# Kernel tuning notes

Measured on AMD Instinct MI355X. Metric: run time of the kernel, lower is better.

Reference implementation:

```python
import jax, jax.numpy as jnp
import numpy as np

DIM = 4096
BATCH = 64
DEFAULT_LR = 0.001
DEFAULT_ALPHA = 0.01
EPS = 1e-08


def setup_inputs() -> dict:
    key = jax.random.key(0)
    k1, k2, k3 = jax.random.split(key, 3)
    weight = jax.random.normal(k1, (DIM, DIM), dtype=jnp.float32)
    input_x = jax.random.normal(k2, (BATCH, DIM), dtype=jnp.float32)
    grad = jax.random.normal(k3, (DIM, DIM), dtype=jnp.float32)
    return {"weight": weight, "input_x": input_x, "grad": grad}


def reference(weight, input_x, grad):
    # L2-normalize inputs along last dim (normalize_inputs=True)
    x = input_x / (jnp.linalg.norm(input_x, axis=-1, keepdims=True) + EPS)
    # batched outer product averaged over batch: (dim, dim)
    outer = jnp.einsum('bi,bj->ij', x, x) / x.shape[0]
    decay_matrix = jnp.eye(DIM, dtype=weight.dtype) - DEFAULT_ALPHA * outer
    # W_{t+1} = W @ (I - alpha * outer) - lr * grad
    new_weight = weight @ decay_matrix - DEFAULT_LR * grad
    return new_weight
```

## Files before the change

kernel.cpp:

```cpp
#include <hip/hip_runtime.h>
#include <math.h>

#define DIM 4096
#define BATCH 64

typedef __attribute__((ext_vector_type(8))) short short8;
typedef __attribute__((ext_vector_type(4))) float f32x4;

__device__ __forceinline__ float4 ld4(const float* p) {
    return *reinterpret_cast<const float4*>(p);
}

__device__ __forceinline__ unsigned short f2bf(float f) {
    unsigned u = __builtin_bit_cast(unsigned, f);
    u = (u + 0x7fffu + ((u >> 16) & 1u)) >> 16;
    return (unsigned short)u;
}

__global__ __launch_bounds__(256) void k_norm(const float* __restrict__ x,
                                              unsigned short* __restrict__ xb1,
                                              unsigned short* __restrict__ xb2) {
    const int b = blockIdx.x;
    const int tid = threadIdx.x;
    const float* row = x + (size_t)b * DIM;

    float ss = 0.f;
    for (int k = tid * 4; k < DIM; k += 256 * 4) {
        float4 v = ld4(row + k);
        ss += v.x * v.x + v.y * v.y + v.z * v.z + v.w * v.w;
    }
#pragma unroll
    for (int m = 32; m >= 1; m >>= 1) ss += __shfl_xor(ss, m, 64);

    __shared__ float wsum[4];
    if ((tid & 63) == 0) wsum[tid >> 6] = ss;
    __syncthreads();
    const float total = wsum[0] + wsum[1] + wsum[2] + wsum[3];
    const float scale = 1.0f / (sqrtf(total) + 1e-8f);

    const int bt = b >> 4;
    const int li = b & 15;
    const int ks = b >> 5;
    const int hi = (b & 31) >> 3;
    const int jr = b & 7;

    for (int k = tid; k < DIM; k += 256) {
        const float v = row[k] * scale;
        const unsigned short h = f2bf(v);
        const int l1 = li | (((k & 31) >> 3) << 4);
        xb1[(size_t)((((bt * 128) + (k >> 5)) * 64 + l1) << 3) + (k & 7)] = h;
        const int l2 = (k & 15) | (hi << 4);
        xb2[(size_t)(((((k >> 4) * 2) + ks) * 64 + l2) << 3) + jr] = h;
    }
}

__global__ __launch_bounds__(1024, 4) void k_fused(const float* __restrict__ W,
                                                   const float* __restrict__ G,
                                                   const unsigned short* __restrict__ xb1,
                                                   const unsigned short* __restrict__ xb2,
                                                   float* __restrict__ out) {
    __shared__ float yp[16 * 4 * 64 * 4];
    __shared__ float y2[16 * 68];

    const int tid = threadIdx.x;
    const int wv = tid >> 6;
    const int l  = tid & 63;
    const int lr = l & 15;
    const int lh = l >> 4;
    const int i0 = blockIdx.x * 16;

    f32x4 acc0 = {0.f, 0.f, 0.f, 0.f};
    f32x4 acc1 = acc0, acc2 = acc0, acc3 = acc0;

    const short8* xb1v = (const short8*)xb1;
#pragma unroll
    for (int kb8 = 0; kb8 < 8; ++kb8) {
        const int kbg = wv * 8 + kb8;
        const float* wp = W + (size_t)(i0 + lr) * DIM + kbg * 32 + lh * 8;
        const float4 wa = ld4(wp);
        const float4 wb = ld4(wp + 4);
        short8 a;
        a[0] = (short)f2bf(wa.x); a[1] = (short)f2bf(wa.y);
        a[2] = (short)f2bf(wa.z); a[3] = (short)f2bf(wa.w);
        a[4] = (short)f2bf(wb.x); a[5] = (short)f2bf(wb.y);
        a[6] = (short)f2bf(wb.z); a[7] = (short)f2bf(wb.w);
        const int bslot = kbg * 64 + l;
        acc0 = __builtin_amdgcn_mfma_f32_16x16x32_bf16(a, xb1v[bslot         ], acc0, 0, 0, 0);
        acc1 = __builtin_amdgcn_mfma_f32_16x16x32_bf16(a, xb1v[bslot + 8192  ], acc1, 0, 0, 0);
        acc2 = __builtin_amdgcn_mfma_f32_16x16x32_bf16(a, xb1v[bslot + 16384 ], acc2, 0, 0, 0);
        acc3 = __builtin_amdgcn_mfma_f32_16x16x32_bf16(a, xb1v[bslot + 24576 ], acc3, 0, 0, 0);
    }
    {
        f32x4* dst = (f32x4*)yp;
        dst[(wv * 4 + 0) * 64 + l] = acc0;
        dst[(wv * 4 + 1) * 64 + l] = acc1;
        dst[(wv * 4 + 2) * 64 + l] = acc2;
        dst[(wv * 4 + 3) * 64 + l] = acc3;
    }
    __syncthreads();

    {
        const int r  = tid >> 6;
        const int bb = tid & 63;
        const int btt = bb >> 4;
        const int lii = (bb & 15) | ((r >> 2) << 4);
        const int jq  = r & 3;
        float s = 0.f;
#pragma unroll
        for (int w = 0; w < 16; ++w) s += yp[((w * 4 + btt) * 64 + lii) * 4 + jq];
        y2[r * 68 + bb] = s;
    }
    __syncthreads();

    const float NC = -0.01f / 64.0f;
    short8 ya0, ya1;
#pragma unroll
    for (int j = 0; j < 8; ++j) {
        ya0[j] = (short)f2bf(NC * y2[lr * 68 + lh * 8 + j]);
        ya1[j] = (short)f2bf(NC * y2[lr * 68 + 32 + lh * 8 + j]);
    }

    constexpr float LRc = 0.001f;
    const short8* xb2v = (const short8*)xb2;
#pragma unroll 4
    for (int t = 0; t < 16; ++t) {
        const int jt = wv * 16 + t;
        const int bslot = jt * 2 * 64 + l;
        f32x4 d = {0.f, 0.f, 0.f, 0.f};
        d = __builtin_amdgcn_mfma_f32_16x16x32_bf16(ya0, xb2v[bslot     ], d, 0, 0, 0);
        d = __builtin_amdgcn_mfma_f32_16x16x32_bf16(ya1, xb2v[bslot + 64], d, 0, 0, 0);
        const size_t base = (size_t)(i0 + lh * 4) * DIM + jt * 16 + lr;
#pragma unroll
        for (int q = 0; q < 4; ++q) {
            const size_t idx = base + (size_t)q * DIM;
            out[idx] = W[idx] - LRc * G[idx] + d[q];
        }
    }
}

extern "C" void kernel_launch(void* const* d_in, const int* in_sizes, int n_in,
                              void* d_out, int out_size, void* d_ws, size_t ws_size,
                              hipStream_t stream) {
    const float* W = (const float*)d_in[0];
    const float* X = (const float*)d_in[1];
    const float* G = (const float*)d_in[2];
    float* out = (float*)d_out;

    unsigned short* xb1 = (unsigned short*)d_ws;
    unsigned short* xb2 = xb1 + (size_t)DIM * BATCH;

    hipLaunchKernelGGL(k_norm, dim3(BATCH), dim3(256), 0, stream, X, xb1, xb2);
    hipLaunchKernelGGL(k_fused, dim3(DIM / 16), dim3(1024), 0, stream,
                       W, G, xb1, xb2, out);
}
```

Baseline: 61.41 us.

## Stage epilogue tiles through LDS for coalesced float4 W/G/out access

The epilogue now writes the MFMA output fragments for each wave to a padded LDS tile. It then reads W and G and writes out as row-contiguous float4 vectors, replacing the scattered scalar accesses of 16 floats per row. This targets poor coalescing on the dominant 3x64MB memory stream. The first GEMM loop also preloads two k-steps of W and xb1 operands ahead of the MFMAs to raise memory-level parallelism. In exchange it adds an extra barrier, an LDS round-trip, and more registers (8 tiles plus 16 float4 loads), which could limit occupancy.

```diff
diff --git a/kernel.cpp b/kernel.cpp
--- a/kernel.cpp
+++ b/kernel.cpp
@@ -59,8 +59,9 @@
                                                    const unsigned short* __restrict__ xb1,
                                                    const unsigned short* __restrict__ xb2,
                                                    float* __restrict__ out) {
-    __shared__ float yp[16 * 4 * 64 * 4];
-    __shared__ float y2[16 * 68];
+    __shared__ __align__(16) float lds[33792];
+    float* yp = lds;
+    float* y2 = lds + 16384;
 
     const int tid = threadIdx.x;
     const int wv = tid >> 6;
@@ -71,24 +72,43 @@
 
     f32x4 acc0 = {0.f, 0.f, 0.f, 0.f};
     f32x4 acc1 = acc0, acc2 = acc0, acc3 = acc0;
-
     const short8* xb1v = (const short8*)xb1;
-#pragma unroll
-    for (int kb8 = 0; kb8 < 8; ++kb8) {
-        const int kbg = wv * 8 + kb8;
+
+#pragma unroll 2
+    for (int s = 0; s < 8; s += 2) {
+        const int kbg = wv * 8 + s;
         const float* wp = W + (size_t)(i0 + lr) * DIM + kbg * 32 + lh * 8;
-        const float4 wa = ld4(wp);
-        const float4 wb = ld4(wp + 4);
-        short8 a;
-        a[0] = (short)f2bf(wa.x); a[1] = (short)f2bf(wa.y);
-        a[2] = (short)f2bf(wa.z); a[3] = (short)f2bf(wa.w);
-        a[4] = (short)f2bf(wb.x); a[5] = (short)f2bf(wb.y);
-        a[6] = (short)f2bf(wb.z); a[7] = (short)f2bf(wb.w);
-        const int bslot = kbg * 64 + l;
-        acc0 = __builtin_amdgcn_mfma_f32_16x16x32_bf16(a, xb1v[bslot         ], acc0, 0, 0, 0);
-        acc1 = __builtin_amdgcn_mfma_f32_16x16x32_bf16(a, xb1v[bslot + 8192  ], acc1, 0, 0, 0);
-        acc2 = __builtin_amdgcn_mfma_f32_16x16x32_bf16(a, xb1v[bslot + 16384 ], acc2, 0, 0, 0);
-        acc3 = __builtin_amdgcn_mfma_f32_16x16x32_bf16(a, xb1v[bslot + 24576 ], acc3, 0, 0, 0);
+        const float4 wa0 = ld4(wp);
+        const float4 wb0 = ld4(wp + 4);
+        const float4 wa1 = ld4(wp + 32);
+        const float4 wb1 = ld4(wp + 36);
+        const int bs0 = kbg * 64 + l;
+        const int bs1 = bs0 + 64;
+        const short8 b00 = xb1v[bs0];
+        const short8 b01 = xb1v[bs0 + 8192];
+        const short8 b02 = xb1v[bs0 + 16384];
+        const short8 b03 = xb1v[bs0 + 24576];
+        const short8 b10 = xb1v[bs1];
+        const short8 b11 = xb1v[bs1 + 8192];
+        const short8 b12 = xb1v[bs1 + 16384];
+        const short8 b13 = xb1v[bs1 + 24576];
+        short8 a0, a1;
+        a0[0] = (short)f2bf(wa0.x); a0[1] = (short)f2bf(wa0.y);
+        a0[2] = (short)f2bf(wa0.z); a0[3] = (short)f2bf(wa0.w);
+        a0[4] = (short)f2bf(wb0.x); a0[5] = (short)f2bf(wb0.y);
+        a0[6] = (short)f2bf(wb0.z); a0[7] = (short)f2bf(wb0.w);
+        a1[0] = (short)f2bf(wa1.x); a1[1] = (short)f2bf(wa1.y);
+        a1[2] = (short)f2bf(wa1.z); a1[3] = (short)f2bf(wa1.w);
+        a1[4] = (short)f2bf(wb1.x); a1[5] = (short)f2bf(wb1.y);
+        a1[6] = (short)f2bf(wb1.z); a1[7] = (short)f2bf(wb1.w);
+        acc0 = __builtin_amdgcn_mfma_f32_16x16x32_bf16(a0, b00, acc0, 0, 0, 0);
+        acc1 = __builtin_amdgcn_mfma_f32_16x16x32_bf16(a0, b01, acc1, 0, 0, 0);
+        acc2 = __builtin_amdgcn_mfma_f32_16x16x32_bf16(a0, b02, acc2, 0, 0, 0);
+        acc3 = __builtin_amdgcn_mfma_f32_16x16x32_bf16(a0, b03, acc3, 0, 0, 0);
+        acc0 = __builtin_amdgcn_mfma_f32_16x16x32_bf16(a1, b10, acc0, 0, 0, 0);
+        acc1 = __builtin_amdgcn_mfma_f32_16x16x32_bf16(a1, b11, acc1, 0, 0, 0);
+        acc2 = __builtin_amdgcn_mfma_f32_16x16x32_bf16(a1, b12, acc2, 0, 0, 0);
+        acc3 = __builtin_amdgcn_mfma_f32_16x16x32_bf16(a1, b13, acc3, 0, 0, 0);
     }
     {
         f32x4* dst = (f32x4*)yp;
@@ -107,7 +127,7 @@
         const int jq  = r & 3;
         float s = 0.f;
 #pragma unroll
-        for (int w = 0; w < 16; ++w) s += yp[((w * 4 + btt) * 64 + lii) * 4 + jq];
+        for (int w = 0; w < 16; ++w) s += yp[(((w * 4 + btt) * 64 + lii) << 2) + jq];
         y2[r * 68 + bb] = s;
     }
     __syncthreads();
@@ -119,21 +139,49 @@
         ya0[j] = (short)f2bf(NC * y2[lr * 68 + lh * 8 + j]);
         ya1[j] = (short)f2bf(NC * y2[lr * 68 + 32 + lh * 8 + j]);
     }
+    __syncthreads();
 
     constexpr float LRc = 0.001f;
     const short8* xb2v = (const short8*)xb2;
-#pragma unroll 4
-    for (int t = 0; t < 16; ++t) {
-        const int jt = wv * 16 + t;
-        const int bslot = jt * 2 * 64 + l;
-        f32x4 d = {0.f, 0.f, 0.f, 0.f};
-        d = __builtin_amdgcn_mfma_f32_16x16x32_bf16(ya0, xb2v[bslot     ], d, 0, 0, 0);
-        d = __builtin_amdgcn_mfma_f32_16x16x32_bf16(ya1, xb2v[bslot + 64], d, 0, 0, 0);
-        const size_t base = (size_t)(i0 + lh * 4) * DIM + jt * 16 + lr;
-#pragma unroll
-        for (int q = 0; q < 4; ++q) {
-            const size_t idx = base + (size_t)q * DIM;
-            out[idx] = W[idx] - LRc * G[idx] + d[q];
+    float* dl = lds + wv * 2112;
+    const int c32 = (l & 31) * 4;
+    const int r0 = l >> 5;
+
+    for (int c = 0; c < 2; ++c) {
+        f32x4 dt[8];
+#pragma unroll
+        for (int tl = 0; tl < 8; ++tl) {
+            const int jt = wv * 16 + c * 8 + tl;
+            const int bslot = jt * 128 + l;
+            f32x4 d = {0.f, 0.f, 0.f, 0.f};
+            d = __builtin_amdgcn_mfma_f32_16x16x32_bf16(ya0, xb2v[bslot], d, 0, 0, 0);
+            d = __builtin_amdgcn_mfma_f32_16x16x32_bf16(ya1, xb2v[bslot + 64], d, 0, 0, 0);
+            dt[tl] = d;
+        }
+#pragma unroll
+        for (int tl = 0; tl < 8; ++tl)
+#pragma unroll
+            for (int q = 0; q < 4; ++q)
+                dl[(lh * 4 + q) * 132 + tl * 16 + lr] = dt[tl][q];
+
+        const int colg = wv * 256 + c * 128 + c32;
+        float4 wv4[8], gv4[8];
+#pragma unroll
+        for (int i = 0; i < 8; ++i) {
+            const size_t gidx = (size_t)(i0 + r0 + 2 * i) * DIM + colg;
+            wv4[i] = ld4(W + gidx);
+            gv4[i] = ld4(G + gidx);
+        }
+#pragma unroll
+        for (int i = 0; i < 8; ++i) {
+            const float4 dd = ld4(dl + (r0 + 2 * i) * 132 + c32);
+            const size_t gidx = (size_t)(i0 + r0 + 2 * i) * DIM + colg;
+            float4 o;
+            o.x = wv4[i].x - LRc * gv4[i].x + dd.x;
+            o.y = wv4[i].y - LRc * gv4[i].y + dd.y;
+            o.z = wv4[i].z - LRc * gv4[i].z + dd.z;
+            o.w = wv4[i].w - LRc * gv4[i].w + dd.w;
+            *reinterpret_cast<float4*>(out + gidx) = o;
         }
     }
 }
```

Result: faster. 58.93 us (-4.0%).

## Swap MFMA operands in epilogue for float4 row stores and truncate W to bf16

Applied to the files above, without the earlier changes.

The second-stage MFMA now has its operands swapped, so each lane holds four consecutive columns of one output row. The W/G loads and out stores in the epilogue become 16-byte float4 accesses instead of strided scalar ones. The W-to-bf16 conversion switches from round-to-nearest-even to plain truncation, packed two at a time. The first loop is only partly unrolled and the B operands are hoisted ahead of the MFMAs. Truncation adds a little precision error in the low-rank correction term.

```diff
diff --git a/kernel.cpp b/kernel.cpp
--- a/kernel.cpp
+++ b/kernel.cpp
@@ -6,6 +6,7 @@
 
 typedef __attribute__((ext_vector_type(8))) short short8;
 typedef __attribute__((ext_vector_type(4))) float f32x4;
+typedef __attribute__((ext_vector_type(4))) unsigned int u32x4;
 
 __device__ __forceinline__ float4 ld4(const float* p) {
     return *reinterpret_cast<const float4*>(p);
@@ -17,9 +18,14 @@
     return (unsigned short)u;
 }
 
+__device__ __forceinline__ unsigned pack_bf2(float x, float y) {
+    return (__builtin_bit_cast(unsigned, x) >> 16) |
+           (__builtin_bit_cast(unsigned, y) & 0xffff0000u);
+}
+
 __global__ __launch_bounds__(256) void k_norm(const float* __restrict__ x,
                                               unsigned short* __restrict__ xb1,
-                                              unsigned short* __restrict__ xb2) {
+                                              unsigned short* __restrict__ xa2) {
     const int b = blockIdx.x;
     const int tid = threadIdx.x;
     const float* row = x + (size_t)b * DIM;
@@ -40,26 +46,26 @@
 
     const int bt = b >> 4;
     const int li = b & 15;
-    const int ks = b >> 5;
-    const int hi = (b & 31) >> 3;
-    const int jr = b & 7;
+    const int ks  = b >> 5;
+    const int bhi = (b >> 3) & 3;
+    const int br  = b & 7;
 
     for (int k = tid; k < DIM; k += 256) {
         const float v = row[k] * scale;
         const unsigned short h = f2bf(v);
         const int l1 = li | (((k & 31) >> 3) << 4);
         xb1[(size_t)((((bt * 128) + (k >> 5)) * 64 + l1) << 3) + (k & 7)] = h;
-        const int l2 = (k & 15) | (hi << 4);
-        xb2[(size_t)(((((k >> 4) * 2) + ks) * 64 + l2) << 3) + jr] = h;
+        const int l2 = (k & 15) | (bhi << 4);
+        xa2[(size_t)(((((k >> 4) * 2) + ks) * 64 + l2) << 3) + br] = h;
     }
 }
 
 __global__ __launch_bounds__(1024, 4) void k_fused(const float* __restrict__ W,
                                                    const float* __restrict__ G,
                                                    const unsigned short* __restrict__ xb1,
-                                                   const unsigned short* __restrict__ xb2,
+                                                   const unsigned short* __restrict__ xa2,
                                                    float* __restrict__ out) {
-    __shared__ float yp[16 * 4 * 64 * 4];
+    __shared__ __align__(16) float yp[16 * 4 * 64 * 4];
     __shared__ float y2[16 * 68];
 
     const int tid = threadIdx.x;
@@ -71,24 +77,29 @@
 
     f32x4 acc0 = {0.f, 0.f, 0.f, 0.f};
     f32x4 acc1 = acc0, acc2 = acc0, acc3 = acc0;
+    const short8* xb1v = (const short8*)xb1;
 
-    const short8* xb1v = (const short8*)xb1;
-#pragma unroll
-    for (int kb8 = 0; kb8 < 8; ++kb8) {
-        const int kbg = wv * 8 + kb8;
+#pragma unroll 2
+    for (int s = 0; s < 8; ++s) {
+        const int kbg = wv * 8 + s;
         const float* wp = W + (size_t)(i0 + lr) * DIM + kbg * 32 + lh * 8;
         const float4 wa = ld4(wp);
         const float4 wb = ld4(wp + 4);
-        short8 a;
-        a[0] = (short)f2bf(wa.x); a[1] = (short)f2bf(wa.y);
-        a[2] = (short)f2bf(wa.z); a[3] = (short)f2bf(wa.w);
-        a[4] = (short)f2bf(wb.x); a[5] = (short)f2bf(wb.y);
-        a[6] = (short)f2bf(wb.z); a[7] = (short)f2bf(wb.w);
-        const int bslot = kbg * 64 + l;
-        acc0 = __builtin_amdgcn_mfma_f32_16x16x32_bf16(a, xb1v[bslot         ], acc0, 0, 0, 0);
-        acc1 = __builtin_amdgcn_mfma_f32_16x16x32_bf16(a, xb1v[bslot + 8192  ], acc1, 0, 0, 0);
-        acc2 = __builtin_amdgcn_mfma_f32_16x16x32_bf16(a, xb1v[bslot + 16384 ], acc2, 0, 0, 0);
-        acc3 = __builtin_amdgcn_mfma_f32_16x16x32_bf16(a, xb1v[bslot + 24576 ], acc3, 0, 0, 0);
+        const int bs = kbg * 64 + l;
+        const short8 b0 = xb1v[bs];
+        const short8 b1 = xb1v[bs + 8192];
+        const short8 b2 = xb1v[bs + 16384];
+        const short8 b3 = xb1v[bs + 24576];
+        u32x4 ap;
+        ap[0] = pack_bf2(wa.x, wa.y);
+        ap[1] = pack_bf2(wa.z, wa.w);
+        ap[2] = pack_bf2(wb.x, wb.y);
+        ap[3] = pack_bf2(wb.z, wb.w);
+        const short8 a = __builtin_bit_cast(short8, ap);
+        acc0 = __builtin_amdgcn_mfma_f32_16x16x32_bf16(a, b0, acc0, 0, 0, 0);
+        acc1 = __builtin_amdgcn_mfma_f32_16x16x32_bf16(a, b1, acc1, 0, 0, 0);
+        acc2 = __builtin_amdgcn_mfma_f32_16x16x32_bf16(a, b2, acc2, 0, 0, 0);
+        acc3 = __builtin_amdgcn_mfma_f32_16x16x32_bf16(a, b3, acc3, 0, 0, 0);
     }
     {
         f32x4* dst = (f32x4*)yp;
@@ -107,7 +118,7 @@
         const int jq  = r & 3;
         float s = 0.f;
 #pragma unroll
-        for (int w = 0; w < 16; ++w) s += yp[((w * 4 + btt) * 64 + lii) * 4 + jq];
+        for (int w = 0; w < 16; ++w) s += yp[(((w * 4 + btt) * 64 + lii) << 2) + jq];
         y2[r * 68 + bb] = s;
     }
     __syncthreads();
@@ -121,20 +132,24 @@
     }
 
     constexpr float LRc = 0.001f;
-    const short8* xb2v = (const short8*)xb2;
+    const short8* xa2v = (const short8*)xa2;
 #pragma unroll 4
     for (int t = 0; t < 16; ++t) {
         const int jt = wv * 16 + t;
-        const int bslot = jt * 2 * 64 + l;
+        const short8 a0 = xa2v[(jt * 2 + 0) * 64 + l];
+        const short8 a1 = xa2v[(jt * 2 + 1) * 64 + l];
         f32x4 d = {0.f, 0.f, 0.f, 0.f};
-        d = __builtin_amdgcn_mfma_f32_16x16x32_bf16(ya0, xb2v[bslot     ], d, 0, 0, 0);
-        d = __builtin_amdgcn_mfma_f32_16x16x32_bf16(ya1, xb2v[bslot + 64], d, 0, 0, 0);
-        const size_t base = (size_t)(i0 + lh * 4) * DIM + jt * 16 + lr;
-#pragma unroll
-        for (int q = 0; q < 4; ++q) {
-            const size_t idx = base + (size_t)q * DIM;
-            out[idx] = W[idx] - LRc * G[idx] + d[q];
-        }
+        d = __builtin_amdgcn_mfma_f32_16x16x32_bf16(a0, ya0, d, 0, 0, 0);
+        d = __builtin_amdgcn_mfma_f32_16x16x32_bf16(a1, ya1, d, 0, 0, 0);
+        const size_t idx = (size_t)(i0 + lr) * DIM + jt * 16 + lh * 4;
+        const float4 w4 = ld4(W + idx);
+        const float4 g4 = ld4(G + idx);
+        float4 o;
+        o.x = w4.x - LRc * g4.x + d[0];
+        o.y = w4.y - LRc * g4.y + d[1];
+        o.z = w4.z - LRc * g4.z + d[2];
+        o.w = w4.w - LRc * g4.w + d[3];
+        *reinterpret_cast<float4*>(out + idx) = o;
     }
 }
 
@@ -147,9 +162,9 @@
     float* out = (float*)d_out;
 
     unsigned short* xb1 = (unsigned short*)d_ws;
-    unsigned short* xb2 = xb1 + (size_t)DIM * BATCH;
+    unsigned short* xa2 = xb1 + (size_t)DIM * BATCH;
 
-    hipLaunchKernelGGL(k_norm, dim3(BATCH), dim3(256), 0, stream, X, xb1, xb2);
+    hipLaunchKernelGGL(k_norm, dim3(BATCH), dim3(256), 0, stream, X, xb1, xa2);
     hipLaunchKernelGGL(k_fused, dim3(DIM / 16), dim3(1024), 0, stream,
-                       W, G, xb1, xb2, out);
+                       W, G, xb1, xa2, out);
 }
```

Result: no change. 61.61 us (+0.3%).

## Stage W and G tiles through LDS with direct global-to-LDS loads for coalescing

Applied to the files above, without the earlier changes.

The first GEMM now loads W rows with async global_load_lds into shared memory. Each wave then reads its A fragment from LDS and converts it with truncating bf16 packing instead of round-to-nearest. The work split changes to 4 batch tiles by 4 k-groups per wave, which shrinks the cross-wave reduction. In the epilogue, W and G are staged through LDS in 512-column chunks and the decay product is written to LDS, so the final output is fully coalesced float4 stores rather than strided scalar accesses. This adds many block-wide barriers and a large LDS footprint, which limits occupancy.

```diff
diff --git a/kernel.cpp b/kernel.cpp
--- a/kernel.cpp
+++ b/kernel.cpp
@@ -6,15 +6,28 @@
 
 typedef __attribute__((ext_vector_type(8))) short short8;
 typedef __attribute__((ext_vector_type(4))) float f32x4;
+typedef __attribute__((ext_vector_type(4))) unsigned int u32x4;
+
+typedef __attribute__((address_space(3))) unsigned int lds_u32;
+typedef const __attribute__((address_space(1))) unsigned int glb_u32;
 
 __device__ __forceinline__ float4 ld4(const float* p) {
     return *reinterpret_cast<const float4*>(p);
+}
+
+__device__ __forceinline__ void gload_lds16(const float* g, float* l) {
+    __builtin_amdgcn_global_load_lds((glb_u32*)g, (lds_u32*)l, 16, 0, 0);
 }
 
 __device__ __forceinline__ unsigned short f2bf(float f) {
     unsigned u = __builtin_bit_cast(unsigned, f);
     u = (u + 0x7fffu + ((u >> 16) & 1u)) >> 16;
     return (unsigned short)u;
+}
+
+__device__ __forceinline__ unsigned pack_bf2(float x, float y) {
+    return (__builtin_bit_cast(unsigned, x) >> 16) |
+           (__builtin_bit_cast(unsigned, y) & 0xffff0000u);
 }
 
 __global__ __launch_bounds__(256) void k_norm(const float* __restrict__ x,
@@ -54,13 +67,18 @@
     }
 }
 
-__global__ __launch_bounds__(1024, 4) void k_fused(const float* __restrict__ W,
-                                                   const float* __restrict__ G,
-                                                   const unsigned short* __restrict__ xb1,
-                                                   const unsigned short* __restrict__ xb2,
-                                                   float* __restrict__ out) {
-    __shared__ float yp[16 * 4 * 64 * 4];
-    __shared__ float y2[16 * 68];
+__global__ __launch_bounds__(1024) void k_fused(const float* __restrict__ W,
+                                                const float* __restrict__ G,
+                                                const unsigned short* __restrict__ xb1,
+                                                const unsigned short* __restrict__ xb2,
+                                                float* __restrict__ out) {
+    __shared__ __align__(16) float lds[24768];
+    float* aw = lds;
+    float* yp = lds + 16448;
+    float* y2 = lds + 20544;
+    float* wg = lds;
+    float* gg = lds + 8256;
+    float* dl = lds + 16512;
 
     const int tid = threadIdx.x;
     const int wv = tid >> 6;
@@ -69,45 +87,54 @@
     const int lh = l >> 4;
     const int i0 = blockIdx.x * 16;
 
-    f32x4 acc0 = {0.f, 0.f, 0.f, 0.f};
-    f32x4 acc1 = acc0, acc2 = acc0, acc3 = acc0;
-
+    const int bt = wv & 3;
+    const int kg = wv >> 2;
     const short8* xb1v = (const short8*)xb1;
-#pragma unroll
-    for (int kb8 = 0; kb8 < 8; ++kb8) {
-        const int kbg = wv * 8 + kb8;
-        const float* wp = W + (size_t)(i0 + lr) * DIM + kbg * 32 + lh * 8;
-        const float4 wa = ld4(wp);
-        const float4 wb = ld4(wp + 4);
-        short8 a;
-        a[0] = (short)f2bf(wa.x); a[1] = (short)f2bf(wa.y);
-        a[2] = (short)f2bf(wa.z); a[3] = (short)f2bf(wa.w);
-        a[4] = (short)f2bf(wb.x); a[5] = (short)f2bf(wb.y);
-        a[6] = (short)f2bf(wb.z); a[7] = (short)f2bf(wb.w);
-        const int bslot = kbg * 64 + l;
-        acc0 = __builtin_amdgcn_mfma_f32_16x16x32_bf16(a, xb1v[bslot         ], acc0, 0, 0, 0);
-        acc1 = __builtin_amdgcn_mfma_f32_16x16x32_bf16(a, xb1v[bslot + 8192  ], acc1, 0, 0, 0);
-        acc2 = __builtin_amdgcn_mfma_f32_16x16x32_bf16(a, xb1v[bslot + 16384 ], acc2, 0, 0, 0);
-        acc3 = __builtin_amdgcn_mfma_f32_16x16x32_bf16(a, xb1v[bslot + 24576 ], acc3, 0, 0, 0);
-    }
-    {
-        f32x4* dst = (f32x4*)yp;
-        dst[(wv * 4 + 0) * 64 + l] = acc0;
-        dst[(wv * 4 + 1) * 64 + l] = acc1;
-        dst[(wv * 4 + 2) * 64 + l] = acc2;
-        dst[(wv * 4 + 3) * 64 + l] = acc3;
-    }
+    f32x4 acc = {0.f, 0.f, 0.f, 0.f};
+
+    for (int ss = 0; ss < 4; ++ss) {
+        {
+            const float* src = W + (size_t)(i0 + wv) * DIM + ss * 1024 + l * 4;
+            float* dst = aw + wv * 1028;
+#pragma unroll
+            for (int qq = 0; qq < 4; ++qq)
+                gload_lds16(src + qq * 256, dst + qq * 256);
+        }
+        __syncthreads();
+
+#pragma unroll
+        for (int i = 0; i < 8; ++i) {
+            const int sl = kg * 8 + i;
+            const float* ap = aw + lr * 1028 + sl * 32 + lh * 8;
+            const float4 a0 = *(const float4*)ap;
+            const float4 a1 = *(const float4*)(ap + 4);
+            u32x4 apk;
+            apk[0] = pack_bf2(a0.x, a0.y);
+            apk[1] = pack_bf2(a0.z, a0.w);
+            apk[2] = pack_bf2(a1.x, a1.y);
+            apk[3] = pack_bf2(a1.z, a1.w);
+            const short8 af = __builtin_bit_cast(short8, apk);
+            const int kstep = ss * 32 + sl;
+            const short8 bf = xb1v[(size_t)bt * 8192 + kstep * 64 + l];
+            acc = __builtin_amdgcn_mfma_f32_16x16x32_bf16(af, bf, acc, 0, 0, 0);
+        }
+        __syncthreads();
+    }
+
+    ((f32x4*)yp)[wv * 64 + l] = acc;
     __syncthreads();
 
     {
         const int r  = tid >> 6;
         const int bb = tid & 63;
+        const int c  = bb & 15;
         const int btt = bb >> 4;
-        const int lii = (bb & 15) | ((r >> 2) << 4);
-        const int jq  = r & 3;
+        const int lsrc = c | ((r >> 2) << 4);
+        const int q = r & 3;
         float s = 0.f;
 #pragma unroll
-        for (int w = 0; w < 16; ++w) s += yp[((w * 4 + btt) * 64 + lii) * 4 + jq];
+        for (int m = 0; m < 4; ++m)
+            s += yp[(btt + 4 * m) * 256 + lsrc * 4 + q];
         y2[r * 68 + bb] = s;
     }
     __syncthreads();
@@ -119,22 +146,53 @@
         ya0[j] = (short)f2bf(NC * y2[lr * 68 + lh * 8 + j]);
         ya1[j] = (short)f2bf(NC * y2[lr * 68 + 32 + lh * 8 + j]);
     }
-
+    __syncthreads();
+
+    const short8* xb2v = (const short8*)xb2;
     constexpr float LRc = 0.001f;
-    const short8* xb2v = (const short8*)xb2;
-#pragma unroll 4
-    for (int t = 0; t < 16; ++t) {
-        const int jt = wv * 16 + t;
-        const int bslot = jt * 2 * 64 + l;
-        f32x4 d = {0.f, 0.f, 0.f, 0.f};
-        d = __builtin_amdgcn_mfma_f32_16x16x32_bf16(ya0, xb2v[bslot     ], d, 0, 0, 0);
-        d = __builtin_amdgcn_mfma_f32_16x16x32_bf16(ya1, xb2v[bslot + 64], d, 0, 0, 0);
-        const size_t base = (size_t)(i0 + lh * 4) * DIM + jt * 16 + lr;
-#pragma unroll
-        for (int q = 0; q < 4; ++q) {
-            const size_t idx = base + (size_t)q * DIM;
-            out[idx] = W[idx] - LRc * G[idx] + d[q];
-        }
+
+    for (int cc = 0; cc < 8; ++cc) {
+        {
+            const size_t rowbase = (size_t)(i0 + wv) * DIM + cc * 512 + l * 4;
+            const float* srcW = W + rowbase;
+            const float* srcG = G + rowbase;
+            float* dstW = wg + wv * 516;
+            float* dstG = gg + wv * 516;
+            gload_lds16(srcW,       dstW);
+            gload_lds16(srcW + 256, dstW + 256);
+            gload_lds16(srcG,       dstG);
+            gload_lds16(srcG + 256, dstG + 256);
+        }
+#pragma unroll
+        for (int t = 0; t < 2; ++t) {
+            const int jl = wv * 2 + t;
+            const int jt = cc * 32 + jl;
+            f32x4 d = {0.f, 0.f, 0.f, 0.f};
+            d = __builtin_amdgcn_mfma_f32_16x16x32_bf16(ya0, xb2v[(size_t)jt * 128 + l], d, 0, 0, 0);
+            d = __builtin_amdgcn_mfma_f32_16x16x32_bf16(ya1, xb2v[(size_t)jt * 128 + 64 + l], d, 0, 0, 0);
+#pragma unroll
+            for (int q = 0; q < 4; ++q)
+                dl[(lh * 4 + q) * 516 + jl * 16 + lr] = d[q];
+        }
+        __syncthreads();
+
+        {
+            const size_t obase = (size_t)(i0 + wv) * DIM + cc * 512 + l * 4;
+            const int lb = wv * 516 + l * 4;
+#pragma unroll
+            for (int h = 0; h < 2; ++h) {
+                const float4 w4 = *(const float4*)(wg + lb + h * 256);
+                const float4 g4 = *(const float4*)(gg + lb + h * 256);
+                const float4 d4 = *(const float4*)(dl + lb + h * 256);
+                float4 o;
+                o.x = w4.x - LRc * g4.x + d4.x;
+                o.y = w4.y - LRc * g4.y + d4.y;
+                o.z = w4.z - LRc * g4.z + d4.z;
+                o.w = w4.w - LRc * g4.w + d4.w;
+                *(float4*)(out + obase + h * 256) = o;
+            }
+        }
+        __syncthreads();
     }
 }
 
@@ -150,6 +208,6 @@
     unsigned short* xb2 = xb1 + (size_t)DIM * BATCH;
 
     hipLaunchKernelGGL(k_norm, dim3(BATCH), dim3(256), 0, stream, X, xb1, xb2);
-    hipLaunchKernelGGL(k_fused, dim3(DIM / 16), dim3(1024), 0, stream,
+    hipLaunchKernelGGL(k_fused, dim3(256), dim3(1024), 0, stream,
                        W, G, xb1, xb2, out);
 }
```

Result: slower. 85.44 us (+39.1%).
